# Performance work log

Hardware: AMD Instinct MI355X
Metric: run time of the kernel (lower is better)

The kernel has to match this reference:

```python
import jax, jax.numpy as jnp
import numpy as np

IMG = 84
CH = 64
OUT = 5
PARAM_KEYS = ['w0', 'b0', 'w1', 'b1', 'w2', 'b2', 'w3', 'b3', 'fc_w', 'fc_b']


def _conv(x, w, b):
    # x: [C,H,W], w: [O,I,3,3] -> [O,H,W] (SAME padding, stride 1)
    y = jax.lax.conv_general_dilated(x[None], w, (1, 1), 'SAME',
                                     dimension_numbers=('NCHW', 'OIHW', 'NCHW'))[0]
    return y + b[:, None, None]


def _pool(x):
    # 2x2 max pool, VALID (84->42->21->10->5)
    return jax.lax.reduce_window(x, -jnp.inf, jax.lax.max, (1, 2, 2), (1, 2, 2), 'VALID')


def _fnet_single(params, x):
    # x: flat [3*84*84] -> logits [OUT]; mirrors fnet_single(params, x) on unsqueezed input
    h = x.reshape(3, IMG, IMG)
    for i in range(4):
        h = _pool(jax.nn.relu(_conv(h, params['w%d' % i], params['b%d' % i])))
    h = h.reshape(-1)  # [CH*5*5]
    return params['fc_w'] @ h + params['fc_b']


def setup_inputs() -> dict:
    key = jax.random.key(0)
    ks = jax.random.split(key, 16)
    N = 64
    x1 = jax.random.normal(ks[0], (N, 3 * IMG * IMG), jnp.float32)
    x2 = jax.random.normal(ks[1], (N, 3 * IMG * IMG), jnp.float32)
    params = {}
    cin = 3
    for i in range(4):
        fan_in = cin * 9
        params['w%d' % i] = jax.random.normal(ks[2 + i], (CH, cin, 3, 3), jnp.float32) * (2.0 / fan_in) ** 0.5
        params['b%d' % i] = jnp.zeros((CH,), jnp.float32)
        cin = CH
    feat = CH * 5 * 5
    params['fc_w'] = jax.random.normal(ks[6], (OUT, feat), jnp.float32) * (1.0 / feat) ** 0.5
    params['fc_b'] = jnp.zeros((OUT,), jnp.float32)
    scalings = jax.random.uniform(ks[7], (len(PARAM_KEYS),), jnp.float32, 0.5, 1.5)
    inp = {'x1': x1, 'x2': x2, 'scalings': scalings, 'c': 2}
    inp.update(params)
    return inp


def reference(x1, x2, w0, b0, w1, b1, w2, b2, w3, b3, fc_w, fc_b, scalings, c):
    params = {'w0': w0, 'b0': b0, 'w1': w1, 'b1': b1, 'w2': w2, 'b2': b2,
              'w3': w3, 'b3': b3, 'fc_w': fc_w, 'fc_b': fc_b}
    jac_fn = jax.vmap(jax.jacrev(_fnet_single), in_axes=(None, 0))
    jac1 = jac_fn(params, x1)  # dict: [N, OUT, *param_shape]
    jac2 = jac_fn(params, x2)  # dict: [M, OUT, *param_shape]
    N, M = x1.shape[0], x2.shape[0]
    K = jnp.zeros((N, M, OUT), x1.dtype)
    for idx, k in enumerate(PARAM_KEYS):  # fixed small loop over parameter tensors
        j1 = (scalings[idx] * jac1[k]).reshape(N, OUT, -1)
        j2 = (scalings[idx] * jac2[k]).reshape(M, OUT, -1)
        K = K + jnp.einsum('Naf,Maf->NMa', j1, j2)
    return K[:, :, c]  # [N, M]
```

## Files before the change

### kernel.cpp

```cpp
#include <hip/hip_runtime.h>
#include <cstdint>

constexpr int OFF_W1 = 0;
constexpr int OFF_B1 = 1728;
constexpr int OFF_W2 = 1792;
constexpr int OFF_B2 = 38656;
constexpr int OFF_W3 = 38720;
constexpr int OFF_B3 = 75584;
constexpr int OFF_W4 = 75648;
constexpr int OFF_B4 = 112512;
constexpr int OFF_H  = 112576;
constexpr int PJ     = 114176;

__global__ __launch_bounds__(256) void k_transpose(
    const float* __restrict__ x1, const float* __restrict__ x2, float* __restrict__ xT)
{
    __shared__ float tile[32][33];
    const int c0 = blockIdx.x * 32, s0 = blockIdx.y * 32;
    const int tx = threadIdx.x, ty = threadIdx.y;
#pragma unroll
    for (int k = 0; k < 4; ++k) {
        const int row = s0 + ty + k * 8;
        const int col = c0 + tx;
        const float* src = (row < 64) ? (x1 + (size_t)row * 21168)
                                      : (x2 + (size_t)(row - 64) * 21168);
        tile[ty + k * 8][tx] = (col < 21168) ? src[col] : 0.f;
    }
    __syncthreads();
#pragma unroll
    for (int k = 0; k < 4; ++k) {
        const int c = c0 + ty + k * 8;
        if (c < 21168) xT[(size_t)c * 128 + (s0 + tx)] = tile[tx][ty + k * 8];
    }
}

__global__ __launch_bounds__(256) void k_wprep(
    const float* __restrict__ w1, const float* __restrict__ w2,
    const float* __restrict__ w3, const float* __restrict__ w4,
    float* __restrict__ wS1, float* __restrict__ wS2, float* __restrict__ wS3,
    float* __restrict__ wS4, float* __restrict__ wB2, float* __restrict__ wB3,
    float* __restrict__ wB4)
{
    const int idx = blockIdx.x * 256 + threadIdx.x;
    if (idx >= 36864) return;
    const int o = idx / 576, rem = idx % 576, i = rem / 9, t = rem % 9;
    wS2[(i * 9 + t) * 64 + o] = w2[idx];
    wS3[(i * 9 + t) * 64 + o] = w3[idx];
    wS4[(i * 9 + t) * 64 + o] = w4[idx];
    wB2[(o * 9 + (8 - t)) * 64 + i] = w2[idx];
    wB3[(o * 9 + (8 - t)) * 64 + i] = w3[idx];
    wB4[(o * 9 + (8 - t)) * 64 + i] = w4[idx];
    if (idx < 1728) {
        const int o1 = idx / 27, r1 = idx % 27, i1 = r1 / 9, t1 = r1 % 9;
        wS1[(i1 * 9 + t1) * 64 + o1] = w1[idx];
    }
}

template<int CIN, int TIN, int OB, int SI, int SY, int SX>
__global__ __launch_bounds__(256) void k_fwd(
    const float* __restrict__ in, const float* __restrict__ wS,
    const float* __restrict__ bias, float* __restrict__ pout,
    unsigned char* __restrict__ mout)
{
    constexpr int PW = TIN / 2;
    const int lane = threadIdx.x;
    const int x0 = blockIdx.x * 4;
    const int o0 = blockIdx.y * OB;
    const int pr = blockIdx.z * 2 + threadIdx.y;
    if (pr >= PW) return;
    const int cr0 = 2 * pr;

    float acc[OB][2][4];
#pragma unroll
    for (int j = 0; j < OB; ++j)
#pragma unroll
        for (int r = 0; r < 2; ++r)
#pragma unroll
            for (int p = 0; p < 4; ++p) acc[j][r][p] = 0.f;

#pragma unroll 1
    for (int i = 0; i < CIN; ++i) {
        float a[4][6];
#pragma unroll
        for (int rr = 0; rr < 4; ++rr) {
            const int y = cr0 - 1 + rr;
            const bool rok = (unsigned)y < (unsigned)TIN;
#pragma unroll
            for (int cc = 0; cc < 6; ++cc) {
                const int x = x0 - 1 + cc;
                a[rr][cc] = (rok && (unsigned)x < (unsigned)TIN)
                    ? in[(size_t)i * SI + (size_t)y * SY + (size_t)x * SX + lane] : 0.f;
            }
        }
        const float* wrow = wS + (i * 9) * 64 + o0;
#pragma unroll
        for (int t = 0; t < 9; ++t) {
            const int dy = t / 3, dx = t % 3;
#pragma unroll
            for (int j = 0; j < OB; ++j) {
                const float wv = wrow[t * 64 + j];
#pragma unroll
                for (int r = 0; r < 2; ++r)
#pragma unroll
                    for (int p = 0; p < 4; ++p)
                        acc[j][r][p] = fmaf(wv, a[r + dy][p + dx], acc[j][r][p]);
            }
        }
    }
#pragma unroll
    for (int j = 0; j < OB; ++j) {
        const float b = bias[o0 + j];
#pragma unroll
        for (int q = 0; q < 2; ++q) {
            const int wx = x0 / 2 + q;
            if (wx >= PW) continue;
            const float c00 = fmaxf(acc[j][0][2 * q]     + b, 0.f);
            const float c01 = fmaxf(acc[j][0][2 * q + 1] + b, 0.f);
            const float c10 = fmaxf(acc[j][1][2 * q]     + b, 0.f);
            const float c11 = fmaxf(acc[j][1][2 * q + 1] + b, 0.f);
            float best = c00; int idx = 0;
            if (c01 > best) { best = c01; idx = 1; }
            if (c10 > best) { best = c10; idx = 2; }
            if (c11 > best) { best = c11; idx = 3; }
            const size_t oi = ((size_t)(pr * PW + wx) * 64 + (o0 + j)) * 128 + lane;
            pout[oi] = best;
            mout[oi] = (unsigned char)(idx | (best > 0.f ? 4 : 0));
        }
    }
}

__global__ __launch_bounds__(128) void k_seed(
    const float* __restrict__ fcw, const int* __restrict__ cptr,
    const float* __restrict__ p4, const float* __restrict__ scal_,
    float* __restrict__ g4, float* __restrict__ JT)
{
    const int s = threadIdx.x;
    const int cell = blockIdx.x / 64, o = blockIdx.x % 64;
    const int c = *cptr;
    const int j = o * 25 + cell;
    const size_t base = ((size_t)cell * 64 + o) * 128 + s;
    g4[base] = fcw[(size_t)c * 1600 + j];
    JT[(size_t)(OFF_H + j) * 128 + s] = scal_[8] * p4[base];
}

template<int TL, int TP, int OB>
__global__ __launch_bounds__(256) void k_bwd(
    const float* __restrict__ gl, const unsigned char* __restrict__ ml,
    const float* __restrict__ wB, float* __restrict__ gout)
{
    const int lane = threadIdx.x;
    const int x0 = blockIdx.x * 4;
    const int i0 = blockIdx.y * OB;
    const int row = blockIdx.z * 2 + threadIdx.y;
    if (row >= TP) return;

    const int prA = (row - 1) >> 1;
    const int prB = (row + 1) >> 1;
    const int pc0 = (x0 - 1) >> 1;
    const int rpar = row & 1;
    const int ridx1 = rpar ? 0 : 1;

    float acc[OB][4];
#pragma unroll
    for (int j = 0; j < OB; ++j)
#pragma unroll
        for (int p = 0; p < 4; ++p) acc[j][p] = 0.f;

#pragma unroll 1
    for (int o = 0; o < 64; ++o) {
        int   mv[2][4];
        float gv[2][4];
#pragma unroll
        for (int r2 = 0; r2 < 2; ++r2) {
            const int prr = r2 ? prB : prA;
            const bool rok = (unsigned)prr < (unsigned)TL;
#pragma unroll
            for (int c2 = 0; c2 < 4; ++c2) {
                const int pcc = pc0 + c2;
                const bool ok = rok && (unsigned)pcc < (unsigned)TL;
                if (ok) {
                    const size_t base = ((size_t)(prr * TL + pcc) * 64 + o) * 128 + lane;
                    mv[r2][c2] = ml[base];
                    gv[r2][c2] = gl[base];
                } else {
                    mv[r2][c2] = 255;
                    gv[r2][c2] = 0.f;
                }
            }
        }
        float a[3][6];
#pragma unroll
        for (int rr = 0; rr < 3; ++rr) {
            const int ridx = (rr == 0) ? 0 : ((rr == 2) ? 1 : ridx1);
            const int ycode = 4 | (((row - 1 + rr) & 1) << 1);
#pragma unroll
            for (int cc = 0; cc < 6; ++cc) {
                const int cidx = (cc + 1) >> 1;
                const int code = ycode | ((cc + 1) & 1);
                a[rr][cc] = (mv[ridx][cidx] == code) ? gv[ridx][cidx] : 0.f;
            }
        }
        const float* wrow = wB + (o * 9) * 64 + i0;
#pragma unroll
        for (int t = 0; t < 9; ++t) {
            const int dy = t / 3, dx = t % 3;
#pragma unroll
            for (int j = 0; j < OB; ++j) {
                const float wv = wrow[t * 64 + j];
#pragma unroll
                for (int p = 0; p < 4; ++p)
                    acc[j][p] = fmaf(wv, a[dy][p + dx], acc[j][p]);
            }
        }
    }
#pragma unroll
    for (int j = 0; j < OB; ++j)
#pragma unroll
        for (int p = 0; p < 4; ++p) {
            const int x = x0 + p;
            if (x < TP)
                gout[((size_t)(row * TP + x) * 64 + (i0 + j)) * 128 + lane] = acc[j][p];
        }
}

template<int TL, int TIN>
__global__ __launch_bounds__(128) void k_wgrad(
    const float* __restrict__ gl, const unsigned char* __restrict__ ml,
    const float* __restrict__ h, const float* __restrict__ scal_,
    const int scalIdx, const int joff, float* __restrict__ JT, const int ychunk)
{
    const int s = threadIdx.x;
    const int o0 = blockIdx.x * 2, i0 = blockIdx.y * 2;
    const int y0 = blockIdx.z * ychunk;
    const int y1 = (y0 + ychunk < TIN) ? y0 + ychunk : TIN;

    float acc[2][2][9];
#pragma unroll
    for (int a = 0; a < 2; ++a)
#pragma unroll
        for (int b = 0; b < 2; ++b)
#pragma unroll
            for (int t = 0; t < 9; ++t) acc[a][b][t] = 0.f;

#pragma unroll 1
    for (int y = y0; y < y1; ++y) {
        const int wy = y >> 1;
        const int ybit = (y & 1) << 1;
        float hw[2][3][3];
#pragma unroll
        for (int ji = 0; ji < 2; ++ji)
#pragma unroll
            for (int dy = 0; dy < 3; ++dy) {
                const int ry = y + dy - 1;
                const bool rok = (unsigned)ry < (unsigned)TIN;
                hw[ji][dy][2] = 0.f;
                hw[ji][dy][1] = 0.f;
                hw[ji][dy][0] = rok ? h[((size_t)(ry * TIN) * 64 + i0 + ji) * 128 + s] : 0.f;
            }
#pragma unroll 1
        for (int xb = 0; xb < ((TIN + 2) / 3) * 3; xb += 3) {
#pragma unroll
            for (int k = 0; k < 3; ++k) {
                const int x = xb + k;
                const int xn = x + 1;
                const bool cok = xn < TIN;
#pragma unroll
                for (int ji = 0; ji < 2; ++ji)
#pragma unroll
                    for (int dy = 0; dy < 3; ++dy) {
                        const int ry = y + dy - 1;
                        hw[ji][dy][(k + 1) % 3] =
                            (cok && (unsigned)ry < (unsigned)TIN)
                                ? h[((size_t)(ry * TIN + xn) * 64 + i0 + ji) * 128 + s] : 0.f;
                    }
                if (x < TIN) {
                    const int wx = x >> 1;
                    const bool uok = (wy < TL) && (wx < TL);
                    const int code = 4 | ybit | (x & 1);
                    float u[2] = {0.f, 0.f};
                    if (uok) {
#pragma unroll
                        for (int jo = 0; jo < 2; ++jo) {
                            const size_t base = ((size_t)(wy * TL + wx) * 64 + o0 + jo) * 128 + s;
                            const int mv = ml[base];
                            const float gv = gl[base];
                            u[jo] = (mv == code) ? gv : 0.f;
                        }
                    }
#pragma unroll
                    for (int jo = 0; jo < 2; ++jo)
#pragma unroll
                        for (int ji = 0; ji < 2; ++ji)
#pragma unroll
                            for (int dy = 0; dy < 3; ++dy)
#pragma unroll
                                for (int dx = 0; dx < 3; ++dx)
                                    acc[jo][ji][dy * 3 + dx] =
                                        fmaf(u[jo], hw[ji][dy][(k + dx + 2) % 3],
                                             acc[jo][ji][dy * 3 + dx]);
                }
            }
        }
    }
    const float sc = scal_[scalIdx];
#pragma unroll
    for (int jo = 0; jo < 2; ++jo)
#pragma unroll
        for (int ji = 0; ji < 2; ++ji)
#pragma unroll
            for (int t = 0; t < 9; ++t) {
                const int feat = joff + ((o0 + jo) * 64 + (i0 + ji)) * 9 + t;
                atomicAdd(&JT[(size_t)feat * 128 + s], sc * acc[jo][ji][t]);
            }
}

__global__ __launch_bounds__(128) void k_wgrad1(
    const float* __restrict__ g1, const unsigned char* __restrict__ m1,
    const float* __restrict__ xT, const float* __restrict__ scal_,
    float* __restrict__ JT)
{
    const int s = threadIdx.x;
    const int o0 = blockIdx.x * 2;
    const int wy = blockIdx.y;

    float acc[2][3][9];
#pragma unroll
    for (int oo = 0; oo < 2; ++oo)
#pragma unroll
        for (int i = 0; i < 3; ++i)
#pragma unroll
            for (int t = 0; t < 9; ++t) acc[oo][i][t] = 0.f;

    float hw[3][4][3];
#pragma unroll
    for (int i = 0; i < 3; ++i)
#pragma unroll
        for (int r = 0; r < 4; ++r) {
            const int ry = 2 * wy - 1 + r;
            hw[i][r][2] = 0.f;
            hw[i][r][1] = 0.f;
            hw[i][r][0] = ((unsigned)ry < 84u)
                ? xT[((size_t)i * 7056 + ry * 84) * 128 + s] : 0.f;
        }
    const int cellrow = wy * 42;

#pragma unroll 1
    for (int xb = 0; xb < 84; xb += 3) {
#pragma unroll
        for (int k = 0; k < 3; ++k) {
            const int x = xb + k;
            const int xn = x + 1;
            const bool cok = xn < 84;
#pragma unroll
            for (int i = 0; i < 3; ++i)
#pragma unroll
                for (int r = 0; r < 4; ++r) {
                    const int ry = 2 * wy - 1 + r;
                    hw[i][r][(k + 1) % 3] = (cok && (unsigned)ry < 84u)
                        ? xT[((size_t)i * 7056 + ry * 84 + xn) * 128 + s] : 0.f;
                }
            const int wx = x >> 1;
            const int xbit = x & 1;
            float u[2][2];
#pragma unroll
            for (int oo = 0; oo < 2; ++oo) {
                const size_t base = ((size_t)(cellrow + wx) * 64 + o0 + oo) * 128 + s;
                const int mv = m1[base];
                const float gv = g1[base];
                u[oo][0] = (mv == (4 | 0 | xbit)) ? gv : 0.f;
                u[oo][1] = (mv == (4 | 2 | xbit)) ? gv : 0.f;
            }
#pragma unroll
            for (int oo = 0; oo < 2; ++oo)
#pragma unroll
                for (int yy = 0; yy < 2; ++yy)
#pragma unroll
                    for (int i = 0; i < 3; ++i)
#pragma unroll
                        for (int dy = 0; dy < 3; ++dy)
#pragma unroll
                            for (int dx = 0; dx < 3; ++dx)
                                acc[oo][i][dy * 3 + dx] =
                                    fmaf(u[oo][yy], hw[i][yy + dy][(k + dx + 2) % 3],
                                         acc[oo][i][dy * 3 + dx]);
        }
    }
    const float sc = scal_[0];
#pragma unroll
    for (int oo = 0; oo < 2; ++oo)
#pragma unroll
        for (int i = 0; i < 3; ++i)
#pragma unroll
            for (int t = 0; t < 9; ++t)
                atomicAdd(&JT[(size_t)(OFF_W1 + (o0 + oo) * 27 + i * 9 + t) * 128 + s],
                          sc * acc[oo][i][t]);
}

__global__ __launch_bounds__(128) void k_dbpart(
    const float* __restrict__ g1, const float* __restrict__ g2,
    const float* __restrict__ g3, const float* __restrict__ g4,
    const unsigned char* __restrict__ m1, const unsigned char* __restrict__ m2,
    const unsigned char* __restrict__ m3, const unsigned char* __restrict__ m4,
    float* __restrict__ part)
{
    const int s = threadIdx.x;
    const int o = blockIdx.x, chunk = blockIdx.y, layer = blockIdx.z;
    const float* g; const unsigned char* m; int nc;
    if (layer == 0)      { g = g1; m = m1; nc = 1764; }
    else if (layer == 1) { g = g2; m = m2; nc = 441; }
    else if (layer == 2) { g = g3; m = m3; nc = 100; }
    else                 { g = g4; m = m4; nc = 25; }
    const int c0 = chunk * nc / 4, c1 = (chunk + 1) * nc / 4;
    float acc = 0.f;
    for (int cell = c0; cell < c1; ++cell) {
        const size_t base = ((size_t)cell * 64 + o) * 128 + s;
        acc += (m[base] & 4) ? g[base] : 0.f;
    }
    part[((size_t)(layer * 4 + chunk) * 64 + o) * 128 + s] = acc;
}

__global__ __launch_bounds__(256) void k_dbred(
    const float* __restrict__ part, const float* __restrict__ scal_,
    float* __restrict__ JT)
{
    const int idx = blockIdx.x * 256 + threadIdx.x;
    const int layer = idx >> 13, o = (idx >> 7) & 63, s = idx & 127;
    float v = 0.f;
#pragma unroll
    for (int ch = 0; ch < 4; ++ch)
        v += part[((size_t)(layer * 4 + ch) * 64 + o) * 128 + s];
    const int offb[4] = {OFF_B1, OFF_B2, OFF_B3, OFF_B4};
    JT[(size_t)(offb[layer] + o) * 128 + s] = scal_[2 * layer + 1] * v;
}

constexpr int NTK_BLOCKS = 446;
__global__ __launch_bounds__(256) void k_ntk(const float* __restrict__ JT,
                                             float* __restrict__ part)
{
    __shared__ float As[32][64], Bs[32][64];
    const int tx = threadIdx.x, ty = threadIdx.y;
    const int t = ty * 16 + tx;
    float acc[4][4];
#pragma unroll
    for (int a = 0; a < 4; ++a)
#pragma unroll
        for (int b = 0; b < 4; ++b) acc[a][b] = 0.f;

    for (int ch = 0; ch < 8; ++ch) {
        const int k0 = (blockIdx.x * 8 + ch) * 32;
        __syncthreads();
#pragma unroll
        for (int q = 0; q < 4; ++q) {
            const int fidx = q * 256 + t;
            const int row = fidx >> 5;
            const int c4 = (fidx & 31) * 4;
            const float4 v = *(const float4*)&JT[(size_t)(k0 + row) * 128 + c4];
            if (c4 < 64) *(float4*)&As[row][c4] = v;
            else         *(float4*)&Bs[row][c4 - 64] = v;
        }
        __syncthreads();
#pragma unroll
        for (int k = 0; k < 32; ++k) {
            const float4 av = *(const float4*)&As[k][ty * 4];
            const float4 bv = *(const float4*)&Bs[k][tx * 4];
            acc[0][0] = fmaf(av.x, bv.x, acc[0][0]);
            acc[0][1] = fmaf(av.x, bv.y, acc[0][1]);
            acc[0][2] = fmaf(av.x, bv.z, acc[0][2]);
            acc[0][3] = fmaf(av.x, bv.w, acc[0][3]);
            acc[1][0] = fmaf(av.y, bv.x, acc[1][0]);
            acc[1][1] = fmaf(av.y, bv.y, acc[1][1]);
            acc[1][2] = fmaf(av.y, bv.z, acc[1][2]);
            acc[1][3] = fmaf(av.y, bv.w, acc[1][3]);
            acc[2][0] = fmaf(av.z, bv.x, acc[2][0]);
            acc[2][1] = fmaf(av.z, bv.y, acc[2][1]);
            acc[2][2] = fmaf(av.z, bv.z, acc[2][2]);
            acc[2][3] = fmaf(av.z, bv.w, acc[2][3]);
            acc[3][0] = fmaf(av.w, bv.x, acc[3][0]);
            acc[3][1] = fmaf(av.w, bv.y, acc[3][1]);
            acc[3][2] = fmaf(av.w, bv.z, acc[3][2]);
            acc[3][3] = fmaf(av.w, bv.w, acc[3][3]);
        }
    }
#pragma unroll
    for (int a = 0; a < 4; ++a)
#pragma unroll
        for (int b = 0; b < 4; ++b)
            part[(size_t)blockIdx.x * 4096 + (ty * 4 + a) * 64 + (tx * 4 + b)] = acc[a][b];
}

__global__ __launch_bounds__(256) void k_ntkred(
    const float* __restrict__ part, const float* __restrict__ scal_,
    float* __restrict__ out)
{
    const int t = blockIdx.x * 256 + threadIdx.x;
    float v = scal_[9] * scal_[9];
    for (int ck = 0; ck < NTK_BLOCKS; ++ck) v += part[(size_t)ck * 4096 + t];
    out[t] = v;
}

extern "C" void kernel_launch(void* const* d_in, const int* in_sizes, int n_in,
                              void* d_out, int out_size, void* d_ws, size_t ws_size,
                              hipStream_t stream)
{
    const void* IN[14];
    if (n_in >= 14 && in_sizes[2] == 10 && in_sizes[3] == 1) {
        for (int k = 0; k < 14; ++k) IN[k] = d_in[k];
    } else {
        IN[0] = d_in[0]; IN[1] = d_in[1];
        IN[2] = d_in[12]; IN[3] = d_in[13];
        for (int k = 0; k < 8; ++k) IN[4 + k] = d_in[2 + k];
        IN[12] = d_in[10]; IN[13] = d_in[11];
    }
    const float* x1   = (const float*)IN[0];
    const float* x2   = (const float*)IN[1];
    const float* scal = (const float*)IN[2];
    const int*   cp   = (const int*)IN[3];
    const float* w1 = (const float*)IN[4];  const float* b1 = (const float*)IN[5];
    const float* w2 = (const float*)IN[6];  const float* b2 = (const float*)IN[7];
    const float* w3 = (const float*)IN[8];  const float* b3 = (const float*)IN[9];
    const float* w4 = (const float*)IN[10]; const float* b4 = (const float*)IN[11];
    const float* fcw = (const float*)IN[12];
    float* out = (float*)d_out;

    char* base = (char*)d_ws;
    size_t off = 0;
    auto alloc = [&](size_t bytes) -> char* {
        char* p = base + off;
        off = (off + bytes + 255) & ~(size_t)255;
        return p;
    };
    float* JT = (float*)alloc((size_t)PJ * 128 * 4);
    float* xT = JT + (size_t)OFF_W3 * 128;
    float* p1 = (float*)alloc((size_t)1764 * 64 * 128 * 4);
    float* p2 = (float*)alloc((size_t)441  * 64 * 128 * 4);
    float* p3 = (float*)alloc((size_t)100  * 64 * 128 * 4);
    float* p4 = (float*)alloc((size_t)25   * 64 * 128 * 4);
    unsigned char* m1 = (unsigned char*)alloc((size_t)1764 * 64 * 128);
    unsigned char* m2 = (unsigned char*)alloc((size_t)441  * 64 * 128);
    unsigned char* m3 = (unsigned char*)alloc((size_t)100  * 64 * 128);
    unsigned char* m4 = (unsigned char*)alloc((size_t)25   * 64 * 128);
    float* g1 = (float*)alloc((size_t)1764 * 64 * 128 * 4);
    float* g2 = (float*)alloc((size_t)441  * 64 * 128 * 4);
    float* g3 = (float*)alloc((size_t)100  * 64 * 128 * 4);
    float* g4 = (float*)alloc((size_t)25   * 64 * 128 * 4);
    float* wS1 = (float*)alloc(1728 * 4);
    float* wS2 = (float*)alloc(36864 * 4);
    float* wS3 = (float*)alloc(36864 * 4);
    float* wS4 = (float*)alloc(36864 * 4);
    float* wB2 = (float*)alloc(36864 * 4);
    float* wB3 = (float*)alloc(36864 * 4);
    float* wB4 = (float*)alloc(36864 * 4);
    float* dbp = (float*)alloc((size_t)16 * 64 * 128 * 4);
    float* ntkp = g1;
    (void)ws_size;

    hipMemsetAsync(JT, 0, (size_t)OFF_B2 * 128 * 4, stream);
    hipMemsetAsync(JT + (size_t)OFF_W4 * 128, 0, (size_t)36864 * 128 * 4, stream);

    k_transpose<<<dim3(662, 4), dim3(32, 8), 0, stream>>>(x1, x2, xT);
    k_wprep<<<144, 256, 0, stream>>>(w1, w2, w3, w4, wS1, wS2, wS3, wS4, wB2, wB3, wB4);

    k_fwd<3, 84, 4, 84 * 84 * 128, 84 * 128, 128>
        <<<dim3(21, 16, 21), dim3(128, 2), 0, stream>>>(xT, wS1, b1, p1, m1);
    k_fwd<64, 42, 4, 128, 42 * 64 * 128, 64 * 128>
        <<<dim3(11, 16, 11), dim3(128, 2), 0, stream>>>(p1, wS2, b2, p2, m2);
    k_fwd<64, 21, 4, 128, 21 * 64 * 128, 64 * 128>
        <<<dim3(5, 16, 5), dim3(128, 2), 0, stream>>>(p2, wS3, b3, p3, m3);
    k_fwd<64, 10, 4, 128, 10 * 64 * 128, 64 * 128>
        <<<dim3(3, 16, 3), dim3(128, 2), 0, stream>>>(p3, wS4, b4, p4, m4);

    k_seed<<<1600, 128, 0, stream>>>(fcw, cp, p4, scal, g4, JT);

    k_bwd<5, 10, 8><<<dim3(3, 8, 5),  dim3(128, 2), 0, stream>>>(g4, m4, wB4, g3);
    k_bwd<10, 21, 8><<<dim3(6, 8, 11), dim3(128, 2), 0, stream>>>(g3, m3, wB3, g2);
    k_bwd<21, 42, 8><<<dim3(11, 8, 21), dim3(128, 2), 0, stream>>>(g2, m2, wB2, g1);

    k_wgrad<5, 10><<<dim3(32, 32, 2), 128, 0, stream>>>(g4, m4, p3, scal, 6, OFF_W4, JT, 5);
    k_wgrad1<<<dim3(32, 42), 128, 0, stream>>>(g1, m1, xT, scal, JT);
    hipMemsetAsync(JT + (size_t)OFF_W3 * 128, 0, (size_t)36864 * 128 * 4, stream);
    k_wgrad<10, 21><<<dim3(32, 32, 3), 128, 0, stream>>>(g3, m3, p2, scal, 4, OFF_W3, JT, 7);
    k_wgrad<21, 42><<<dim3(32, 32, 6), 128, 0, stream>>>(g2, m2, p1, scal, 2, OFF_W2, JT, 7);

    k_dbpart<<<dim3(64, 4, 4), 128, 0, stream>>>(g1, g2, g3, g4, m1, m2, m3, m4, dbp);
    k_dbred<<<128, 256, 0, stream>>>(dbp, scal, JT);

    k_ntk<<<NTK_BLOCKS, dim3(16, 16), 0, stream>>>(JT, ntkp);
    k_ntkred<<<16, 256, 0, stream>>>(ntkp, scal, out);
}
```

Measured before the change: 2.263 ms.

## Restructure weight-gradient loop over pooled cells with 4x4 sliding input window

The weight-gradient kernel now iterates over pooled output positions instead of individual input pixels. It loads each gradient/mask pair once per pooled cell and expands it into the four possible argmax positions. The input activations are held in a 4x4 register window that slides two columns at a time. This cuts redundant global loads of gradients, masks and activations, at the cost of more live registers, and the z-chunk sizes are retuned to pooled rows.

```diff
diff --git a/kernel.cpp b/kernel.cpp
--- a/kernel.cpp
+++ b/kernel.cpp
@@ -227,12 +227,12 @@
 __global__ __launch_bounds__(128) void k_wgrad(
     const float* __restrict__ gl, const unsigned char* __restrict__ ml,
     const float* __restrict__ h, const float* __restrict__ scal_,
-    const int scalIdx, const int joff, float* __restrict__ JT, const int ychunk)
+    const int scalIdx, const int joff, float* __restrict__ JT, const int wychunk)
 {
     const int s = threadIdx.x;
     const int o0 = blockIdx.x * 2, i0 = blockIdx.y * 2;
-    const int y0 = blockIdx.z * ychunk;
-    const int y1 = (y0 + ychunk < TIN) ? y0 + ychunk : TIN;
+    const int wy0 = blockIdx.z * wychunk;
+    const int wy1 = (wy0 + wychunk < TL) ? wy0 + wychunk : TL;
 
     float acc[2][2][9];
 #pragma unroll
@@ -243,52 +243,43 @@
             for (int t = 0; t < 9; ++t) acc[a][b][t] = 0.f;
 
 #pragma unroll 1
-    for (int y = y0; y < y1; ++y) {
-        const int wy = y >> 1;
-        const int ybit = (y & 1) << 1;
-        float hw[2][3][3];
+    for (int wy = wy0; wy < wy1; ++wy) {
+        float hw[2][4][4];
 #pragma unroll
         for (int ji = 0; ji < 2; ++ji)
 #pragma unroll
-            for (int dy = 0; dy < 3; ++dy) {
-                const int ry = y + dy - 1;
+            for (int r = 0; r < 4; ++r) {
+                const int ry = 2 * wy - 1 + r;
                 const bool rok = (unsigned)ry < (unsigned)TIN;
-                hw[ji][dy][2] = 0.f;
-                hw[ji][dy][1] = 0.f;
-                hw[ji][dy][0] = rok ? h[((size_t)(ry * TIN) * 64 + i0 + ji) * 128 + s] : 0.f;
+                hw[ji][r][0] = 0.f;
+#pragma unroll
+                for (int c = 1; c < 4; ++c) {
+                    const int col = c - 1;
+                    hw[ji][r][c] = rok
+                        ? h[((size_t)(ry * TIN + col) * 64 + i0 + ji) * 128 + s] : 0.f;
+                }
             }
 #pragma unroll 1
-        for (int xb = 0; xb < ((TIN + 2) / 3) * 3; xb += 3) {
-#pragma unroll
-            for (int k = 0; k < 3; ++k) {
-                const int x = xb + k;
-                const int xn = x + 1;
-                const bool cok = xn < TIN;
-#pragma unroll
-                for (int ji = 0; ji < 2; ++ji)
-#pragma unroll
-                    for (int dy = 0; dy < 3; ++dy) {
-                        const int ry = y + dy - 1;
-                        hw[ji][dy][(k + 1) % 3] =
-                            (cok && (unsigned)ry < (unsigned)TIN)
-                                ? h[((size_t)(ry * TIN + xn) * 64 + i0 + ji) * 128 + s] : 0.f;
-                    }
-                if (x < TIN) {
-                    const int wx = x >> 1;
-                    const bool uok = (wy < TL) && (wx < TL);
-                    const int code = 4 | ybit | (x & 1);
-                    float u[2] = {0.f, 0.f};
-                    if (uok) {
-#pragma unroll
-                        for (int jo = 0; jo < 2; ++jo) {
-                            const size_t base = ((size_t)(wy * TL + wx) * 64 + o0 + jo) * 128 + s;
-                            const int mv = ml[base];
-                            const float gv = gl[base];
-                            u[jo] = (mv == code) ? gv : 0.f;
-                        }
-                    }
-#pragma unroll
-                    for (int jo = 0; jo < 2; ++jo)
+        for (int wx = 0; wx < TL; ++wx) {
+            float uu[2][2][2];
+#pragma unroll
+            for (int jo = 0; jo < 2; ++jo) {
+                const size_t base = ((size_t)(wy * TL + wx) * 64 + o0 + jo) * 128 + s;
+                const int mv = ml[base];
+                const float gv = gl[base];
+#pragma unroll
+                for (int yy = 0; yy < 2; ++yy)
+#pragma unroll
+                    for (int xx = 0; xx < 2; ++xx)
+                        uu[jo][yy][xx] = (mv == (4 | (yy << 1) | xx)) ? gv : 0.f;
+            }
+#pragma unroll
+            for (int jo = 0; jo < 2; ++jo)
+#pragma unroll
+                for (int yy = 0; yy < 2; ++yy)
+#pragma unroll
+                    for (int xx = 0; xx < 2; ++xx) {
+                        const float uv = uu[jo][yy][xx];
 #pragma unroll
                         for (int ji = 0; ji < 2; ++ji)
 #pragma unroll
@@ -296,8 +287,30 @@
 #pragma unroll
                                 for (int dx = 0; dx < 3; ++dx)
                                     acc[jo][ji][dy * 3 + dx] =
-                                        fmaf(u[jo], hw[ji][dy][(k + dx + 2) % 3],
+                                        fmaf(uv, hw[ji][yy + dy][xx + dx],
                                              acc[jo][ji][dy * 3 + dx]);
+                    }
+            if (wx + 1 < TL) {
+#pragma unroll
+                for (int ji = 0; ji < 2; ++ji)
+#pragma unroll
+                    for (int r = 0; r < 4; ++r) {
+                        hw[ji][r][0] = hw[ji][r][2];
+                        hw[ji][r][1] = hw[ji][r][3];
+                    }
+#pragma unroll
+                for (int c = 2; c < 4; ++c) {
+                    const int col = 2 * wx + 1 + c;
+                    const bool cok = col < TIN;
+#pragma unroll
+                    for (int ji = 0; ji < 2; ++ji)
+#pragma unroll
+                        for (int r = 0; r < 4; ++r) {
+                            const int ry = 2 * wy - 1 + r;
+                            hw[ji][r][c] = (cok && (unsigned)ry < (unsigned)TIN)
+                                ? h[((size_t)(ry * TIN + col) * 64 + i0 + ji) * 128 + s]
+                                : 0.f;
+                        }
                 }
             }
         }
@@ -575,11 +588,11 @@
     k_bwd<10, 21, 8><<<dim3(6, 8, 11), dim3(128, 2), 0, stream>>>(g3, m3, wB3, g2);
     k_bwd<21, 42, 8><<<dim3(11, 8, 21), dim3(128, 2), 0, stream>>>(g2, m2, wB2, g1);
 
-    k_wgrad<5, 10><<<dim3(32, 32, 2), 128, 0, stream>>>(g4, m4, p3, scal, 6, OFF_W4, JT, 5);
+    k_wgrad<5, 10><<<dim3(32, 32, 2), 128, 0, stream>>>(g4, m4, p3, scal, 6, OFF_W4, JT, 3);
     k_wgrad1<<<dim3(32, 42), 128, 0, stream>>>(g1, m1, xT, scal, JT);
     hipMemsetAsync(JT + (size_t)OFF_W3 * 128, 0, (size_t)36864 * 128 * 4, stream);
-    k_wgrad<10, 21><<<dim3(32, 32, 3), 128, 0, stream>>>(g3, m3, p2, scal, 4, OFF_W3, JT, 7);
-    k_wgrad<21, 42><<<dim3(32, 32, 6), 128, 0, stream>>>(g2, m2, p1, scal, 2, OFF_W2, JT, 7);
+    k_wgrad<10, 21><<<dim3(32, 32, 3), 128, 0, stream>>>(g3, m3, p2, scal, 4, OFF_W3, JT, 4);
+    k_wgrad<21, 42><<<dim3(32, 32, 6), 128, 0, stream>>>(g2, m2, p1, scal, 2, OFF_W2, JT, 4);
 
     k_dbpart<<<dim3(64, 4, 4), 128, 0, stream>>>(g1, g2, g3, g4, m1, m2, m3, m4, dbp);
     k_dbred<<<128, 256, 0, stream>>>(dbp, scal, JT);
```

Result: faster. 2.214 ms (-2.2%).
